# Optimization experiments

Hardware: AMD Instinct MI355X
Metric: run time of the kernel (lower is better)

## Reference

```python
import jax, jax.numpy as jnp
import numpy as np

NH, NP = 8, 4  # num_heads, num_points (num_levels = 1)


def setup_inputs() -> dict:
    key = jax.random.key(0)
    bs, nq, E = 8, 64 * 64, 256
    ks = jax.random.split(key, 9)
    s = 1.0 / np.sqrt(E)
    inp = {
        "query": jax.random.normal(ks[0], (bs, nq, E), dtype=jnp.float32),
        "value_w": jax.random.uniform(ks[1], (E, E), jnp.float32, -s, s),
        "value_b": jax.random.uniform(ks[2], (E,), jnp.float32, -s, s),
        "off_w": jax.random.uniform(ks[3], (NH * NP * 2, E), jnp.float32, -s, s),
        "off_b": jax.random.uniform(ks[4], (NH * NP * 2,), jnp.float32, -1.0, 1.0),
        "attn_w": jax.random.uniform(ks[5], (NH * NP, E), jnp.float32, -s, s),
        "attn_b": jax.random.uniform(ks[6], (NH * NP,), jnp.float32, -s, s),
        "out_w": jax.random.uniform(ks[7], (E, E), jnp.float32, -s, s),
        "out_b": jax.random.uniform(ks[8], (E,), jnp.float32, -s, s),
    }
    return inp


def _msda(query, value_w, value_b, off_w, off_b, attn_w, attn_b, out_w, out_b):
    bs, nq, E = query.shape
    hd = E // NH
    H = int(round(np.sqrt(nq)))
    W = H
    # reference points: meshgrid('ij') over linspace(0,1,H); stacked (col, row) = (x, y)
    r = np.linspace(0.0, 1.0, H, dtype=np.float32)
    row, col = np.meshgrid(r, r, indexing="ij")
    ref = jnp.asarray(np.stack([col, row], -1).reshape(-1, 2))  # (nq, 2)

    # projections (torch Linear convention: y = x @ W.T + b)
    value = jnp.einsum("bqe,fe->bqf", query, value_w) + value_b
    v = value.reshape(bs, nq, NH, hd).transpose(0, 2, 1, 3).reshape(bs * NH, H * W, hd)

    off = (jnp.einsum("bqe,fe->bqf", query, off_w) + off_b).reshape(bs, nq, NH, NP, 2)
    attn = jax.nn.softmax(
        (jnp.einsum("bqe,fe->bqf", query, attn_w) + attn_b).reshape(bs, nq, NH, NP),
        axis=-1,
    )

    norm = jnp.array([W, H], dtype=query.dtype)  # offset_normalizer = (w, h)
    loc = ref[None, :, None, None, :] + off / norm  # (bs, nq, nh, np, 2) in [0,1]
    # grid_sample bilinear, align_corners=False: pixel = loc * size - 0.5
    px = (loc[..., 0] * W - 0.5).transpose(0, 2, 1, 3).reshape(bs * NH, nq * NP)
    py = (loc[..., 1] * H - 0.5).transpose(0, 2, 1, 3).reshape(bs * NH, nq * NP)

    x0 = jnp.floor(px)
    y0 = jnp.floor(py)
    wx = px - x0
    wy = py - y0
    x0i = x0.astype(jnp.int32)
    y0i = y0.astype(jnp.int32)

    out = jnp.zeros((bs * NH, nq * NP, hd), dtype=query.dtype)
    for dy, dx in ((0, 0), (0, 1), (1, 0), (1, 1)):
        xi = x0i + dx
        yi = y0i + dy
        w = (wx if dx else 1.0 - wx) * (wy if dy else 1.0 - wy)
        valid = (xi >= 0) & (xi < W) & (yi >= 0) & (yi < H)  # zero padding
        idx = jnp.clip(yi, 0, H - 1) * W + jnp.clip(xi, 0, W - 1)
        g = jnp.take_along_axis(v, idx[..., None], axis=1)
        out = out + g * (w * valid)[..., None]

    out = out.reshape(bs, NH, nq, NP, hd)
    out = jnp.einsum("bhqpd,bhqp->bqhd", out, attn.transpose(0, 2, 1, 3)).reshape(bs, nq, E)
    out = jnp.einsum("bqe,fe->bqf", out, out_w) + out_b
    # mmcv MSDA adds identity (query) internally; wrapper adds residual again
    return out + 2.0 * query


def reference(query, value_w, value_b, off_w, off_b, attn_w, attn_b, out_w, out_b):
    return _msda(query, value_w, value_b, off_w, off_b, attn_w, attn_b, out_w, out_b)
```

## Files before the change

kernel.cpp:

```cpp
#include <hip/hip_runtime.h>
#include <hip/hip_bf16.h>
#include <math.h>

#define BS 8
#define NQ 4096
#define E  256
#define NH 8
#define NP 4
#define HD 32
#define GW 64
#define GH 64
#define T  (BS * NQ)
#define NPAD 384
#define MSTR 96

typedef __attribute__((ext_vector_type(8))) short bf16x8;
typedef __attribute__((ext_vector_type(4))) float f32x4;
typedef __attribute__((ext_vector_type(8))) unsigned short u16x8;

__device__ __forceinline__ float b2f(unsigned short u) {
    union { unsigned int i; float f; } x; x.i = ((unsigned int)u) << 16; return x.f;
}
__device__ __forceinline__ unsigned short f2b(float f) {
    __hip_bfloat16 h = __float2bfloat16(f);
    return *reinterpret_cast<unsigned short*>(&h);
}
__device__ __forceinline__ void gload16(const void* g, void* l) {
    __builtin_amdgcn_global_load_lds(
        (__attribute__((address_space(1))) void*)g,
        (__attribute__((address_space(3))) void*)l, 16, 0, 0);
}


__global__ __launch_bounds__(256) void prep_weights(
    const float* __restrict__ vw, const float* __restrict__ vb,
    const float* __restrict__ ow, const float* __restrict__ ob,
    const float* __restrict__ aw, const float* __restrict__ ab,
    const float* __restrict__ outw,
    unsigned short* __restrict__ Wcat, unsigned short* __restrict__ Wo,
    float* __restrict__ bcat)
{
    int i = blockIdx.x * 256 + threadIdx.x;
    if (i < NPAD * E) {
        int n = i >> 8, k = i & 255;
        float w = 0.f;
        if      (n < 256) w = vw[n * E + k];
        else if (n < 320) w = ow[(n - 256) * E + k];
        else if (n < 352) w = aw[(n - 320) * E + k];
        Wcat[i] = f2b(w);
    } else {
        int j = i - NPAD * E;
        if (j < E * E) Wo[j] = f2b(outw[j]);
    }
    if (i < NPAD) {
        float bv = 0.f;
        if      (i < 256) bv = vb[i];
        else if (i < 320) bv = ob[i - 256];
        else if (i < 352) bv = ab[i - 320];
        bcat[i] = bv;
    }
}

__global__ __launch_bounds__(512) void gemm_proj(
    const float* __restrict__ Aq,
    const unsigned short* __restrict__ W,
    const float* __restrict__ bias,
    unsigned short* __restrict__ Vt,
    unsigned short* __restrict__ Mt)
{
    __shared__ __align__(16) unsigned short ldsA[4096];
    __shared__ __align__(16) unsigned short ldsB[24576];

    const int tid  = threadIdx.x;
    const int lane = tid & 63;
    const int wave = tid >> 6;
    const int wm   = wave >> 2;
    const int wn   = wave & 3;
    const int bm   = blockIdx.x * 64;
    const int lrow = lane & 15, lchunk = lane >> 4;

    f32x4 acc[2][6] = {};

    for (int k0 = 0; k0 < 256; k0 += 64) {
#pragma unroll
        for (int p = 0; p < 6; ++p) {
            int g = p * 512 + tid;
            int row = g >> 3;
            int c = (g & 7) ^ (row & 7);
            gload16(W + (size_t)row * 256 + k0 + c * 8, &ldsB[(size_t)g * 8]);
        }
        {
            int row = tid >> 3;
            int c = (tid & 7) ^ (row & 7);
            const float* ap = Aq + (size_t)(bm + row) * 256 + k0 + c * 8;
            float4 f0 = *(const float4*)(ap + 0);
            float4 f1 = *(const float4*)(ap + 4);
            u16x8 o;
            o[0]=f2b(f0.x); o[1]=f2b(f0.y); o[2]=f2b(f0.z); o[3]=f2b(f0.w);
            o[4]=f2b(f1.x); o[5]=f2b(f1.y); o[6]=f2b(f1.z); o[7]=f2b(f1.w);
            *(u16x8*)&ldsA[(size_t)tid * 8] = o;
        }
        __syncthreads();

#pragma unroll
        for (int kk = 0; kk < 2; ++kk) {
            const int C = kk * 4 + lchunk;
            bf16x8 af[2], bfr[6];
#pragma unroll
            for (int m = 0; m < 2; ++m) {
                int row = wm * 32 + m * 16 + lrow;
                af[m] = *(const bf16x8*)&ldsA[(size_t)(row * 8 + (C ^ (row & 7))) * 8];
            }
#pragma unroll
            for (int n = 0; n < 6; ++n) {
                int row = wn * 96 + n * 16 + lrow;
                bfr[n] = *(const bf16x8*)&ldsB[(size_t)(row * 8 + (C ^ (row & 7))) * 8];
            }
#pragma unroll
            for (int m = 0; m < 2; ++m)
#pragma unroll
                for (int n = 0; n < 6; ++n)
                    acc[m][n] = __builtin_amdgcn_mfma_f32_16x16x32_bf16(
                        af[m], bfr[n], acc[m][n], 0, 0, 0);
        }
        __syncthreads();
    }

    const int orow0 = (lane >> 4) * 4;
    const int ocol  = lane & 15;
#pragma unroll
    for (int n = 0; n < 6; ++n) {
        int colg = wn * 96 + n * 16 + ocol;
        if (colg >= 352) continue;
        float bv = bias[colg];
#pragma unroll
        for (int m = 0; m < 2; ++m) {
#pragma unroll
            for (int r = 0; r < 4; ++r) {
                int rowg = bm + wm * 32 + m * 16 + orow0 + r;
                unsigned short v = f2b(acc[m][n][r] + bv);
                if (colg < 256) {
                    int b = rowg >> 12, q = rowg & 4095;
                    int h = colg >> 5, ch = colg & 31;
                    Vt[((size_t)(((b << 3) + h) << 12) + q) * 32 + ch] = v;
                } else if (colg < 320) {
                    Mt[(size_t)rowg * MSTR + (colg - 256)] = v;
                } else {
                    Mt[(size_t)rowg * MSTR + 64 + (colg - 320)] = v;
                }
            }
        }
    }
}

__global__ __launch_bounds__(256) void sample_kernel(
    const unsigned short* __restrict__ Vt,
    const unsigned short* __restrict__ Mt,
    unsigned short* __restrict__ S)
{
    const int blk = ((blockIdx.x & 7) << 9) + (blockIdx.x >> 3);
    const int gid = blk * 256 + threadIdx.x;
    const int d0 = gid & 3;
    const int h  = (gid >> 2) & 7;
    const int t  = gid >> 5;
    const int b  = t >> 12;
    const int q  = t & 4095;

    const float refx = (float)(q & 63) * (64.0f / 63.0f);
    const float refy = (float)(q >> 6) * (64.0f / 63.0f);

    const unsigned short* __restrict__ mrow = Mt + (size_t)t * MSTR;
    u16x8  offv = *(const u16x8*)&mrow[h * 8];
    ushort4 lg  = *(const ushort4*)&mrow[64 + h * 4];

    float l0 = b2f(lg.x), l1 = b2f(lg.y), l2 = b2f(lg.z), l3 = b2f(lg.w);
    float m = fmaxf(fmaxf(l0, l1), fmaxf(l2, l3));
    float e0 = __expf(l0 - m), e1 = __expf(l1 - m);
    float e2 = __expf(l2 - m), e3 = __expf(l3 - m);
    float inv = 1.0f / (e0 + e1 + e2 + e3);
    float at[4] = {e0 * inv, e1 * inv, e2 * inv, e3 * inv};

    const unsigned short* __restrict__ vbase =
        Vt + ((size_t)(((b << 3) + h) << 12)) * 32 + d0 * 8;

    float acc[8] = {};
#pragma unroll
    for (int p = 0; p < NP; ++p) {
        float ox = b2f(offv[2 * p]);
        float oy = b2f(offv[2 * p + 1]);
        float px = refx + ox - 0.5f;
        float py = refy + oy - 0.5f;
        float fx = floorf(px), fy = floorf(py);
        int x0 = (int)fx, y0 = (int)fy;
        float wx = px - fx, wy = py - fy;
        float a = at[p];

        int x1 = x0 + 1, y1 = y0 + 1;
        float vx0 = (x0 >= 0 && x0 < GW) ? 1.f : 0.f;
        float vx1 = (x1 >= 0 && x1 < GW) ? 1.f : 0.f;
        float vy0 = (y0 >= 0 && y0 < GH) ? 1.f : 0.f;
        float vy1 = (y1 >= 0 && y1 < GH) ? 1.f : 0.f;

        float w00 = (1.f - wx) * (1.f - wy) * a * vx0 * vy0;
        float w10 = wx * (1.f - wy) * a * vx1 * vy0;
        float w01 = (1.f - wx) * wy * a * vx0 * vy1;
        float w11 = wx * wy * a * vx1 * vy1;

        int x0c = min(max(x0, 0), GW - 1), x1c = min(max(x1, 0), GW - 1);
        int y0c = min(max(y0, 0), GH - 1), y1c = min(max(y1, 0), GH - 1);

        u16x8 g00 = *(const u16x8*)&vbase[(size_t)(y0c * GW + x0c) * 32];
        u16x8 g10 = *(const u16x8*)&vbase[(size_t)(y0c * GW + x1c) * 32];
        u16x8 g01 = *(const u16x8*)&vbase[(size_t)(y1c * GW + x0c) * 32];
        u16x8 g11 = *(const u16x8*)&vbase[(size_t)(y1c * GW + x1c) * 32];
#pragma unroll
        for (int j = 0; j < 8; ++j)
            acc[j] += w00 * b2f(g00[j]) + w10 * b2f(g10[j])
                    + w01 * b2f(g01[j]) + w11 * b2f(g11[j]);
    }

    u16x8 o;
#pragma unroll
    for (int j = 0; j < 8; ++j) o[j] = f2b(acc[j]);
    *(u16x8*)&S[(size_t)t * E + h * HD + d0 * 8] = o;
}

__global__ __launch_bounds__(512) void gemm_out(
    const unsigned short* __restrict__ A,
    const unsigned short* __restrict__ W,
    const float* __restrict__ bias,
    const float* __restrict__ resid,
    float* __restrict__ Out)
{
    __shared__ __align__(16) unsigned short ldsA[4096];
    __shared__ __align__(16) unsigned short ldsB[16384];

    const int tid  = threadIdx.x;
    const int lane = tid & 63;
    const int wave = tid >> 6;
    const int wm   = wave >> 2;
    const int wn   = wave & 3;
    const int bm   = blockIdx.x * 64;
    const int lrow = lane & 15, lchunk = lane >> 4;

    f32x4 acc[2][4] = {};

    for (int k0 = 0; k0 < 256; k0 += 64) {
        {
            int row = tid >> 3;
            int c = (tid & 7) ^ (row & 7);
            gload16(A + (size_t)(bm + row) * 256 + k0 + c * 8,
                    &ldsA[(size_t)tid * 8]);
        }
#pragma unroll
        for (int p = 0; p < 4; ++p) {
            int g = p * 512 + tid;
            int row = g >> 3;
            int c = (g & 7) ^ (row & 7);
            gload16(W + (size_t)row * 256 + k0 + c * 8, &ldsB[(size_t)g * 8]);
        }
        __syncthreads();

#pragma unroll
        for (int kk = 0; kk < 2; ++kk) {
            const int C = kk * 4 + lchunk;
            bf16x8 af[2], bfr[4];
#pragma unroll
            for (int m = 0; m < 2; ++m) {
                int row = wm * 32 + m * 16 + lrow;
                af[m] = *(const bf16x8*)&ldsA[(size_t)(row * 8 + (C ^ (row & 7))) * 8];
            }
#pragma unroll
            for (int n = 0; n < 4; ++n) {
                int row = wn * 64 + n * 16 + lrow;
                bfr[n] = *(const bf16x8*)&ldsB[(size_t)(row * 8 + (C ^ (row & 7))) * 8];
            }
#pragma unroll
            for (int m = 0; m < 2; ++m)
#pragma unroll
                for (int n = 0; n < 4; ++n)
                    acc[m][n] = __builtin_amdgcn_mfma_f32_16x16x32_bf16(
                        af[m], bfr[n], acc[m][n], 0, 0, 0);
        }
        __syncthreads();
    }

    const int orow0 = (lane >> 4) * 4;
    const int ocol  = lane & 15;
#pragma unroll
    for (int m = 0; m < 2; ++m) {
#pragma unroll
        for (int n = 0; n < 4; ++n) {
            int colg = wn * 64 + n * 16 + ocol;
            float bv = bias[colg];
#pragma unroll
            for (int r = 0; r < 4; ++r) {
                int rowg = bm + wm * 32 + m * 16 + orow0 + r;
                Out[(size_t)rowg * 256 + colg] =
                    acc[m][n][r] + bv + 2.0f * resid[(size_t)rowg * 256 + colg];
            }
        }
    }
}

extern "C" void kernel_launch(void* const* d_in, const int* in_sizes, int n_in,
                              void* d_out, int out_size, void* d_ws, size_t ws_size,
                              hipStream_t stream)
{
    const float* query   = (const float*)d_in[0];
    const float* value_w = (const float*)d_in[1];
    const float* value_b = (const float*)d_in[2];
    const float* off_w   = (const float*)d_in[3];
    const float* off_b   = (const float*)d_in[4];
    const float* attn_w  = (const float*)d_in[5];
    const float* attn_b  = (const float*)d_in[6];
    const float* out_w   = (const float*)d_in[7];
    const float* out_b   = (const float*)d_in[8];

    char* w = (char*)d_ws;
    unsigned short* Vt   = (unsigned short*)w;  w += (size_t)T * E * 2;
    unsigned short* Mt   = (unsigned short*)w;  w += (size_t)T * MSTR * 2;
    unsigned short* S    = (unsigned short*)w;  w += (size_t)T * E * 2;
    unsigned short* Wcat = (unsigned short*)w;  w += (size_t)NPAD * E * 2;
    unsigned short* Wo   = (unsigned short*)w;  w += (size_t)E * E * 2;
    float*          bcat = (float*)w;

    prep_weights<<<(NPAD * E + E * E + 255) / 256, 256, 0, stream>>>(
        value_w, value_b, off_w, off_b, attn_w, attn_b, out_w, Wcat, Wo, bcat);

    gemm_proj<<<T / 64, 512, 0, stream>>>(query, Wcat, bcat, Vt, Mt);

    sample_kernel<<<T * 32 / 256, 256, 0, stream>>>(Vt, Mt, S);

    gemm_out<<<T / 64, 512, 0, stream>>>(S, Wo, out_b, query, (float*)d_out);
}
```

Measured before the change: 55.14 us.

## Fuse bilinear sampling into output projection GEMM via shared memory

Merges the sampling kernel with the output GEMM so each block samples 64 tokens across all 8 heads and writes bf16 results straight into LDS as the full-K A tile. This removes the global round trip of the intermediate S buffer and one kernel launch. In exchange, each thread now gathers a full 32-channel head, which cuts thread-level parallelism for the gathers. LDS grows to 64 KB, and the Wo tiles are reloaded serially between k-steps with extra barriers.

```diff
diff --git a/kernel.cpp b/kernel.cpp
--- a/kernel.cpp
+++ b/kernel.cpp
@@ -153,127 +153,131 @@
     }
 }
 
-__global__ __launch_bounds__(256) void sample_kernel(
+__global__ __launch_bounds__(512) void fused_sample_out(
     const unsigned short* __restrict__ Vt,
     const unsigned short* __restrict__ Mt,
-    unsigned short* __restrict__ S)
-{
-    const int blk = ((blockIdx.x & 7) << 9) + (blockIdx.x >> 3);
-    const int gid = blk * 256 + threadIdx.x;
-    const int d0 = gid & 3;
-    const int h  = (gid >> 2) & 7;
-    const int t  = gid >> 5;
-    const int b  = t >> 12;
-    const int q  = t & 4095;
-
-    const float refx = (float)(q & 63) * (64.0f / 63.0f);
-    const float refy = (float)(q >> 6) * (64.0f / 63.0f);
-
-    const unsigned short* __restrict__ mrow = Mt + (size_t)t * MSTR;
-    u16x8  offv = *(const u16x8*)&mrow[h * 8];
-    ushort4 lg  = *(const ushort4*)&mrow[64 + h * 4];
-
-    float l0 = b2f(lg.x), l1 = b2f(lg.y), l2 = b2f(lg.z), l3 = b2f(lg.w);
-    float m = fmaxf(fmaxf(l0, l1), fmaxf(l2, l3));
-    float e0 = __expf(l0 - m), e1 = __expf(l1 - m);
-    float e2 = __expf(l2 - m), e3 = __expf(l3 - m);
-    float inv = 1.0f / (e0 + e1 + e2 + e3);
-    float at[4] = {e0 * inv, e1 * inv, e2 * inv, e3 * inv};
-
-    const unsigned short* __restrict__ vbase =
-        Vt + ((size_t)(((b << 3) + h) << 12)) * 32 + d0 * 8;
-
-    float acc[8] = {};
-#pragma unroll
-    for (int p = 0; p < NP; ++p) {
-        float ox = b2f(offv[2 * p]);
-        float oy = b2f(offv[2 * p + 1]);
-        float px = refx + ox - 0.5f;
-        float py = refy + oy - 0.5f;
-        float fx = floorf(px), fy = floorf(py);
-        int x0 = (int)fx, y0 = (int)fy;
-        float wx = px - fx, wy = py - fy;
-        float a = at[p];
-
-        int x1 = x0 + 1, y1 = y0 + 1;
-        float vx0 = (x0 >= 0 && x0 < GW) ? 1.f : 0.f;
-        float vx1 = (x1 >= 0 && x1 < GW) ? 1.f : 0.f;
-        float vy0 = (y0 >= 0 && y0 < GH) ? 1.f : 0.f;
-        float vy1 = (y1 >= 0 && y1 < GH) ? 1.f : 0.f;
-
-        float w00 = (1.f - wx) * (1.f - wy) * a * vx0 * vy0;
-        float w10 = wx * (1.f - wy) * a * vx1 * vy0;
-        float w01 = (1.f - wx) * wy * a * vx0 * vy1;
-        float w11 = wx * wy * a * vx1 * vy1;
-
-        int x0c = min(max(x0, 0), GW - 1), x1c = min(max(x1, 0), GW - 1);
-        int y0c = min(max(y0, 0), GH - 1), y1c = min(max(y1, 0), GH - 1);
-
-        u16x8 g00 = *(const u16x8*)&vbase[(size_t)(y0c * GW + x0c) * 32];
-        u16x8 g10 = *(const u16x8*)&vbase[(size_t)(y0c * GW + x1c) * 32];
-        u16x8 g01 = *(const u16x8*)&vbase[(size_t)(y1c * GW + x0c) * 32];
-        u16x8 g11 = *(const u16x8*)&vbase[(size_t)(y1c * GW + x1c) * 32];
-#pragma unroll
-        for (int j = 0; j < 8; ++j)
-            acc[j] += w00 * b2f(g00[j]) + w10 * b2f(g10[j])
-                    + w01 * b2f(g01[j]) + w11 * b2f(g11[j]);
-    }
-
-    u16x8 o;
-#pragma unroll
-    for (int j = 0; j < 8; ++j) o[j] = f2b(acc[j]);
-    *(u16x8*)&S[(size_t)t * E + h * HD + d0 * 8] = o;
-}
-
-__global__ __launch_bounds__(512) void gemm_out(
-    const unsigned short* __restrict__ A,
-    const unsigned short* __restrict__ W,
+    const unsigned short* __restrict__ Wo,
     const float* __restrict__ bias,
     const float* __restrict__ resid,
     float* __restrict__ Out)
 {
-    __shared__ __align__(16) unsigned short ldsA[4096];
+    __shared__ __align__(16) unsigned short ldsA[16384];
     __shared__ __align__(16) unsigned short ldsB[16384];
 
+    const int bid = blockIdx.x;
+    const int nb  = ((bid & 7) << 6) + (bid >> 3);
+    const int t0  = nb * 64;
+    const int b   = t0 >> 12;
     const int tid  = threadIdx.x;
     const int lane = tid & 63;
     const int wave = tid >> 6;
-    const int wm   = wave >> 2;
-    const int wn   = wave & 3;
-    const int bm   = blockIdx.x * 64;
+
+#pragma unroll
+    for (int p = 0; p < 4; ++p) {
+        int g = p * 512 + tid;
+        int row = g >> 3;
+        int c = (g & 7) ^ (row & 7);
+        gload16(Wo + (size_t)row * 256 + c * 8, &ldsB[(size_t)g * 8]);
+    }
+
+    {
+        const int h = wave, l = lane;
+        const int t = t0 + l;
+        const int q = t & 4095;
+        const float refx = (float)(q & 63) * (64.0f / 63.0f);
+        const float refy = (float)(q >> 6) * (64.0f / 63.0f);
+
+        const unsigned short* mrow = Mt + (size_t)t * MSTR;
+        u16x8  offv = *(const u16x8*)&mrow[h * 8];
+        ushort4 lg  = *(const ushort4*)&mrow[64 + h * 4];
+
+        float l0 = b2f(lg.x), l1 = b2f(lg.y), l2 = b2f(lg.z), l3 = b2f(lg.w);
+        float m = fmaxf(fmaxf(l0, l1), fmaxf(l2, l3));
+        float e0 = __expf(l0 - m), e1 = __expf(l1 - m);
+        float e2 = __expf(l2 - m), e3 = __expf(l3 - m);
+        float inv = 1.0f / (e0 + e1 + e2 + e3);
+        float at[4] = {e0 * inv, e1 * inv, e2 * inv, e3 * inv};
+
+        const unsigned short* vb0 = Vt + ((size_t)(((b << 3) + h) << 12)) * 32;
+
+#pragma unroll
+        for (int half = 0; half < 2; ++half) {
+            float acc[2][8] = {};
+#pragma unroll
+            for (int p = 0; p < NP; ++p) {
+                float ox = b2f(offv[2 * p]);
+                float oy = b2f(offv[2 * p + 1]);
+                float px = refx + ox - 0.5f;
+                float py = refy + oy - 0.5f;
+                float fx = floorf(px), fy = floorf(py);
+                int x0 = (int)fx, y0 = (int)fy;
+                float wx = px - fx, wy = py - fy;
+                float a = at[p];
+
+                int x1 = x0 + 1, y1 = y0 + 1;
+                float vx0 = (x0 >= 0 && x0 < GW) ? 1.f : 0.f;
+                float vx1 = (x1 >= 0 && x1 < GW) ? 1.f : 0.f;
+                float vy0 = (y0 >= 0 && y0 < GH) ? 1.f : 0.f;
+                float vy1 = (y1 >= 0 && y1 < GH) ? 1.f : 0.f;
+
+                float w00 = (1.f - wx) * (1.f - wy) * a * vx0 * vy0;
+                float w10 = wx * (1.f - wy) * a * vx1 * vy0;
+                float w01 = (1.f - wx) * wy * a * vx0 * vy1;
+                float w11 = wx * wy * a * vx1 * vy1;
+
+                int x0c = min(max(x0, 0), GW - 1), x1c = min(max(x1, 0), GW - 1);
+                int y0c = min(max(y0, 0), GH - 1), y1c = min(max(y1, 0), GH - 1);
+
+#define CORNER(Y, X, WT)                                                      \
+                {                                                             \
+                    const unsigned short* src =                               \
+                        vb0 + (size_t)((Y) * GW + (X)) * 32 + half * 16;      \
+                    u16x8 s0 = *(const u16x8*)(src);                          \
+                    u16x8 s1 = *(const u16x8*)(src + 8);                      \
+                    _Pragma("unroll")                                         \
+                    for (int j = 0; j < 8; ++j) {                             \
+                        acc[0][j] += (WT) * b2f(s0[j]);                       \
+                        acc[1][j] += (WT) * b2f(s1[j]);                       \
+                    }                                                         \
+                }
+                CORNER(y0c, x0c, w00);
+                CORNER(y0c, x1c, w10);
+                CORNER(y1c, x0c, w01);
+                CORNER(y1c, x1c, w11);
+#undef CORNER
+            }
+#pragma unroll
+            for (int jj = 0; jj < 2; ++jj) {
+                u16x8 o;
+#pragma unroll
+                for (int j = 0; j < 8; ++j) o[j] = f2b(acc[jj][j]);
+                int chunk = h * 4 + half * 2 + jj;
+                *(u16x8*)&ldsA[(size_t)(l * 32 + (chunk ^ (l & 7))) * 8] = o;
+            }
+        }
+    }
+    __syncthreads();
+
+    const int wm = wave >> 2, wn = wave & 3;
     const int lrow = lane & 15, lchunk = lane >> 4;
 
     f32x4 acc[2][4] = {};
 
-    for (int k0 = 0; k0 < 256; k0 += 64) {
-        {
-            int row = tid >> 3;
-            int c = (tid & 7) ^ (row & 7);
-            gload16(A + (size_t)(bm + row) * 256 + k0 + c * 8,
-                    &ldsA[(size_t)tid * 8]);
-        }
-#pragma unroll
-        for (int p = 0; p < 4; ++p) {
-            int g = p * 512 + tid;
-            int row = g >> 3;
-            int c = (g & 7) ^ (row & 7);
-            gload16(W + (size_t)row * 256 + k0 + c * 8, &ldsB[(size_t)g * 8]);
-        }
-        __syncthreads();
-
+    for (int ks4 = 0; ks4 < 4; ++ks4) {
 #pragma unroll
         for (int kk = 0; kk < 2; ++kk) {
-            const int C = kk * 4 + lchunk;
+            const int C  = ks4 * 8 + kk * 4 + lchunk;
+            const int Cb = kk * 4 + lchunk;
             bf16x8 af[2], bfr[4];
 #pragma unroll
             for (int m = 0; m < 2; ++m) {
                 int row = wm * 32 + m * 16 + lrow;
-                af[m] = *(const bf16x8*)&ldsA[(size_t)(row * 8 + (C ^ (row & 7))) * 8];
+                af[m] = *(const bf16x8*)&ldsA[(size_t)(row * 32 + (C ^ (row & 7))) * 8];
             }
 #pragma unroll
             for (int n = 0; n < 4; ++n) {
                 int row = wn * 64 + n * 16 + lrow;
-                bfr[n] = *(const bf16x8*)&ldsB[(size_t)(row * 8 + (C ^ (row & 7))) * 8];
+                bfr[n] = *(const bf16x8*)&ldsB[(size_t)(row * 8 + (Cb ^ (row & 7))) * 8];
             }
 #pragma unroll
             for (int m = 0; m < 2; ++m)
@@ -283,6 +287,17 @@
                         af[m], bfr[n], acc[m][n], 0, 0, 0);
         }
         __syncthreads();
+        if (ks4 < 3) {
+#pragma unroll
+            for (int p = 0; p < 4; ++p) {
+                int g = p * 512 + tid;
+                int row = g >> 3;
+                int c = (g & 7) ^ (row & 7);
+                gload16(Wo + (size_t)row * 256 + (ks4 + 1) * 64 + c * 8,
+                        &ldsB[(size_t)g * 8]);
+            }
+            __syncthreads();
+        }
     }
 
     const int orow0 = (lane >> 4) * 4;
@@ -295,7 +310,7 @@
             float bv = bias[colg];
 #pragma unroll
             for (int r = 0; r < 4; ++r) {
-                int rowg = bm + wm * 32 + m * 16 + orow0 + r;
+                int rowg = t0 + wm * 32 + m * 16 + orow0 + r;
                 Out[(size_t)rowg * 256 + colg] =
                     acc[m][n][r] + bv + 2.0f * resid[(size_t)rowg * 256 + colg];
             }
@@ -320,7 +335,6 @@
     char* w = (char*)d_ws;
     unsigned short* Vt   = (unsigned short*)w;  w += (size_t)T * E * 2;
     unsigned short* Mt   = (unsigned short*)w;  w += (size_t)T * MSTR * 2;
-    unsigned short* S    = (unsigned short*)w;  w += (size_t)T * E * 2;
     unsigned short* Wcat = (unsigned short*)w;  w += (size_t)NPAD * E * 2;
     unsigned short* Wo   = (unsigned short*)w;  w += (size_t)E * E * 2;
     float*          bcat = (float*)w;
@@ -330,7 +344,6 @@
 
     gemm_proj<<<T / 64, 512, 0, stream>>>(query, Wcat, bcat, Vt, Mt);
 
-    sample_kernel<<<T * 32 / 256, 256, 0, stream>>>(Vt, Mt, S);
-
-    gemm_out<<<T / 64, 512, 0, stream>>>(S, Wo, out_b, query, (float*)d_out);
-}
+    fused_sample_out<<<T / 64, 512, 0, stream>>>(
+        Vt, Mt, Wo, out_b, query, (float*)d_out);
+}
```

Result: slower. 63.13 us (+14.5%).
